# Kernel optimization log

Hardware: AMD Instinct MI355X
Metric: run time of the kernel (lower is better)

## Reference

```python
import jax, jax.numpy as jnp
import numpy as np
from jax import lax


def _viterbi_decode(logits, trans):
    """Batched Viterbi decode (tf.contrib.crf.crf_decode semantics, full lengths).
    logits: [B, T, U] unary potentials; trans: [U, U], trans[i, j] = score(i -> j).
    Returns int32 tags [B, T]."""
    logits_t = jnp.swapaxes(logits, 0, 1)  # [T, B, U]
    init_v = logits_t[0]                   # [B, U]

    def fwd_step(v, logit_t):
        # scores[b, i, j] = v[b, i] + trans[i, j]
        scores = v[:, :, None] + trans[None, :, :]          # [B, U, U]
        bp = jnp.argmax(scores, axis=1).astype(jnp.int32)   # [B, U] best prev tag
        v_new = jnp.max(scores, axis=1) + logit_t           # [B, U]
        return v_new, bp

    v_last, bps = lax.scan(fwd_step, init_v, logits_t[1:])  # bps: [T-1, B, U]
    last_tag = jnp.argmax(v_last, axis=1).astype(jnp.int32)  # [B]

    def bwd_step(tag, bp):
        # tag is the tag at t+1; bp[b, k] = best tag at t given tag k at t+1
        new_tag = jnp.take_along_axis(bp, tag[:, None], axis=1)[:, 0]
        return new_tag, new_tag

    _, tags_prefix = lax.scan(bwd_step, last_tag, bps, reverse=True)  # [T-1, B]
    tags = jnp.concatenate([tags_prefix, last_tag[None, :]], axis=0)  # [T, B]
    return jnp.swapaxes(tags, 0, 1)  # [B, T]


def setup_inputs() -> dict:
    key = jax.random.key(0)
    k0, k1, k2, k3, k4 = jax.random.split(key, 5)
    B, T, D, U = 64, 512, 1024, 128
    x = jax.random.normal(k0, (B, T, D), dtype=jnp.float32)
    kernel = jax.random.normal(k1, (D, U), dtype=jnp.float32) * (1.0 / np.sqrt(D))
    bias = jnp.zeros((U,), dtype=jnp.float32)
    chain_kernel = jax.random.normal(k2, (U, U), dtype=jnp.float32) * 0.1
    left_boundary = jax.random.normal(k3, (U,), dtype=jnp.float32) * 0.1
    right_boundary = jax.random.normal(k4, (U,), dtype=jnp.float32) * 0.1
    return {
        "x": x,
        "kernel": kernel,
        "bias": bias,
        "chain_kernel": chain_kernel,
        "left_boundary": left_boundary,
        "right_boundary": right_boundary,
    }


def reference(x, kernel, bias, chain_kernel, left_boundary, right_boundary):
    # _dense_layer: linear activation, x @ kernel + bias
    logits = jnp.einsum("btd,du->btu", x, kernel) + bias  # [B, T, U]
    # add_boundary_energy with mask=None: boundaries on first / last timestep
    logits = logits.at[:, 0, :].add(left_boundary)
    logits = logits.at[:, -1, :].add(right_boundary)
    # test_mode='viterbi', learn_mode='join': return decoded tags cast to float32
    tags = _viterbi_decode(logits, chain_kernel)
    return tags.astype(jnp.float32)
```

## Files before the change

kernel.cpp:

```cpp
#include <hip/hip_runtime.h>

#define T_SEQ 512
#define U_TAGS 128
#define D_DIM 1024

__global__ __launch_bounds__(256) void crf_gemm(
    const float* __restrict__ A, const float* __restrict__ Bk,
    const float* __restrict__ bias, const float* __restrict__ lb,
    const float* __restrict__ rb, float* __restrict__ C) {
  __shared__ float As[16][132];
  __shared__ float Bs[16][132];
  const int tid = threadIdx.x;
  const int tx = tid & 15, ty = tid >> 4;
  const int row0 = blockIdx.x * 128;

  const int am = tid >> 2, ak = (tid & 3) << 2;
  const int bk = tid >> 5, bn = (tid & 31) << 2;

  float acc[8][8] = {};

  float4 a0 = *(const float4*)&A[(size_t)(row0 + am) * D_DIM + ak];
  float4 a1 = *(const float4*)&A[(size_t)(row0 + am + 64) * D_DIM + ak];
  float4 b0 = *(const float4*)&Bk[(size_t)bk * U_TAGS + bn];
  float4 b1 = *(const float4*)&Bk[(size_t)(bk + 8) * U_TAGS + bn];

  for (int k0 = 0; k0 < D_DIM; k0 += 16) {
    As[ak + 0][am] = a0.x; As[ak + 1][am] = a0.y;
    As[ak + 2][am] = a0.z; As[ak + 3][am] = a0.w;
    As[ak + 0][am + 64] = a1.x; As[ak + 1][am + 64] = a1.y;
    As[ak + 2][am + 64] = a1.z; As[ak + 3][am + 64] = a1.w;
    *(float4*)&Bs[bk][bn] = b0;
    *(float4*)&Bs[bk + 8][bn] = b1;
    __syncthreads();
    if (k0 + 16 < D_DIM) {
      a0 = *(const float4*)&A[(size_t)(row0 + am) * D_DIM + k0 + 16 + ak];
      a1 = *(const float4*)&A[(size_t)(row0 + am + 64) * D_DIM + k0 + 16 + ak];
      b0 = *(const float4*)&Bk[(size_t)(k0 + 16 + bk) * U_TAGS + bn];
      b1 = *(const float4*)&Bk[(size_t)(k0 + 16 + bk + 8) * U_TAGS + bn];
    }
#pragma unroll
    for (int kk = 0; kk < 16; ++kk) {
      float a[8], b[8];
      *(float4*)&a[0] = *(const float4*)&As[kk][ty * 8];
      *(float4*)&a[4] = *(const float4*)&As[kk][ty * 8 + 4];
      *(float4*)&b[0] = *(const float4*)&Bs[kk][tx * 8];
      *(float4*)&b[4] = *(const float4*)&Bs[kk][tx * 8 + 4];
#pragma unroll
      for (int r = 0; r < 8; ++r)
#pragma unroll
        for (int c = 0; c < 8; ++c) acc[r][c] = fmaf(a[r], b[c], acc[r][c]);
    }
    __syncthreads();
  }

#pragma unroll
  for (int r = 0; r < 8; ++r) {
    const int row = row0 + ty * 8 + r;
    const int t = row & (T_SEQ - 1);
    float o[8];
#pragma unroll
    for (int c = 0; c < 8; ++c) {
      float v = acc[r][c] + bias[tx * 8 + c];
      if (t == 0) v += lb[tx * 8 + c];
      if (t == T_SEQ - 1) v += rb[tx * 8 + c];
      o[c] = v;
    }
    *(float4*)&C[(size_t)row * U_TAGS + tx * 8] = *(float4*)&o[0];
    *(float4*)&C[(size_t)row * U_TAGS + tx * 8 + 4] = *(float4*)&o[4];
  }
}

__device__ __forceinline__ float fmax_dpp1(float m) {
  int i = __builtin_amdgcn_mov_dpp(__float_as_int(m), 0xB1, 0xF, 0xF, true);
  return fmaxf(m, __int_as_float(i));
}
__device__ __forceinline__ float fmax_dpp2(float m) {
  int i = __builtin_amdgcn_mov_dpp(__float_as_int(m), 0x4E, 0xF, 0xF, true);
  return fmaxf(m, __int_as_float(i));
}
__device__ __forceinline__ int imin_dpp1(int v) {
  int i = __builtin_amdgcn_mov_dpp(v, 0xB1, 0xF, 0xF, true);
  return v < i ? v : i;
}
__device__ __forceinline__ int imin_dpp2(int v) {
  int i = __builtin_amdgcn_mov_dpp(v, 0x4E, 0xF, 0xF, true);
  return v < i ? v : i;
}

__global__ __launch_bounds__(512) void crf_viterbi(
    const float* __restrict__ logits,
    const float* __restrict__ trans,
    float* __restrict__ out) {
  __shared__ __align__(16) float vbuf[2][U_TAGS];
  __shared__ __align__(16) unsigned char bp[T_SEQ * U_TAGS];
  __shared__ unsigned char tags[T_SEQ];
  __shared__ float red_v[8];
  __shared__ int red_i[8];

  const int b = blockIdx.x;
  const int tid = threadIdx.x;
  const int j = tid >> 2;
  const int seg = tid & 3;
  const float* lg_b = logits + (size_t)b * T_SEQ * U_TAGS;

  float* tstage = (float*)bp;
#pragma unroll
  for (int it = 0; it < 8; ++it)
    *(float4*)&tstage[(it * 512 + tid) * 4] =
        *(const float4*)&trans[(it * 512 + tid) * 4];
  __syncthreads();
  float tr[32];
#pragma unroll
  for (int e = 0; e < 32; ++e) tr[e] = tstage[(seg * 32 + e) * U_TAGS + j];
  if (tid < U_TAGS) vbuf[0][tid] = lg_b[tid];
  __syncthreads();

  float lg = lg_b[U_TAGS + j];
  for (int t = 1; t < T_SEQ; ++t) {
    float lg_next = (t < T_SEQ - 1) ? lg_b[(size_t)(t + 1) * U_TAGS + j] : 0.0f;
    const float* vcur = &vbuf[(t - 1) & 1][seg * 32];
    float s[32];
#pragma unroll
    for (int q = 0; q < 8; ++q) {
      float4 vv = *(const float4*)&vcur[q * 4];
      s[q * 4 + 0] = vv.x + tr[q * 4 + 0];
      s[q * 4 + 1] = vv.y + tr[q * 4 + 1];
      s[q * 4 + 2] = vv.z + tr[q * 4 + 2];
      s[q * 4 + 3] = vv.w + tr[q * 4 + 3];
    }
    float m0 = s[0], m1 = s[1], m2 = s[2], m3 = s[3];
#pragma unroll
    for (int e = 4; e < 32; e += 4) {
      m0 = fmaxf(m0, s[e + 0]); m1 = fmaxf(m1, s[e + 1]);
      m2 = fmaxf(m2, s[e + 2]); m3 = fmaxf(m3, s[e + 3]);
    }
    float m = fmaxf(fmaxf(m0, m1), fmaxf(m2, m3));
    m = fmax_dpp1(m);
    m = fmax_dpp2(m);
    int el = 64;
#pragma unroll
    for (int e = 31; e >= 0; --e) el = (s[e] == m) ? e : el;
    int ic = (el < 64) ? (seg * 32 + el) : 1023;
    ic = imin_dpp1(ic);
    ic = imin_dpp2(ic);
    if (seg == 0) {
      vbuf[t & 1][j] = m + lg;
      bp[(t - 1) * U_TAGS + j] = (unsigned char)ic;
    }
    __syncthreads();
    lg = lg_next;
  }

  if (tid < U_TAGS) {
    float val = vbuf[(T_SEQ - 1) & 1][tid];
    int idx = tid;
#pragma unroll
    for (int off = 1; off < 64; off <<= 1) {
      float vo = __shfl_xor(val, off);
      int io = __shfl_xor(idx, off);
      if (vo > val || (vo == val && io < idx)) { val = vo; idx = io; }
    }
    if ((tid & 63) == 0) { red_v[tid >> 6] = val; red_i[tid >> 6] = idx; }
  }
  __syncthreads();
  if (tid == 0) {
    int tg = (red_v[1] > red_v[0]) ? red_i[1] : red_i[0];
    tags[T_SEQ - 1] = (unsigned char)tg;
    for (int t = T_SEQ - 2; t >= 0; --t) {
      tg = bp[t * U_TAGS + tg];
      tags[t] = (unsigned char)tg;
    }
  }
  __syncthreads();
  out[(size_t)b * T_SEQ + tid] = (float)tags[tid];
}

extern "C" void kernel_launch(void* const* d_in, const int* in_sizes, int n_in,
                              void* d_out, int out_size, void* d_ws,
                              size_t ws_size, hipStream_t stream) {
  const float* x = (const float*)d_in[0];
  const float* kern = (const float*)d_in[1];
  const float* bias = (const float*)d_in[2];
  const float* chain = (const float*)d_in[3];
  const float* lb = (const float*)d_in[4];
  const float* rb = (const float*)d_in[5];
  float* out = (float*)d_out;
  float* logits = (float*)d_ws;

  crf_gemm<<<256, 256, 0, stream>>>(x, kern, bias, lb, rb, logits);
  crf_viterbi<<<64, 512, 0, stream>>>(logits, chain, out);
}
```

Measured before the change: 614.9 us.

## Parallelize Viterbi backtrack by segments and cut LDS conflicts in recurrence

The serial single-thread backtrack becomes a segmented parallel scheme. Each of 8 waves composes the backpointer maps over its 64-step segment for all 128 tags. The segment seeds are then chained and each segment is replayed in parallel. The forward loop also replicates the score vector per segment to avoid LDS bank conflicts, uses max3 trees and split argmin chains, prefetches logits two steps ahead, and swaps __syncthreads for an LDS-only barrier. The GEMM B-fragment layout is interleaved to reduce shared-memory bank conflicts. The segmented backtrack does 128 times more pointer chasing per segment, and the custom barrier depends on the global loads needing no vmcnt wait.

```diff
diff --git a/kernel.cpp b/kernel.cpp
--- a/kernel.cpp
+++ b/kernel.cpp
@@ -43,8 +43,8 @@
       float a[8], b[8];
       *(float4*)&a[0] = *(const float4*)&As[kk][ty * 8];
       *(float4*)&a[4] = *(const float4*)&As[kk][ty * 8 + 4];
-      *(float4*)&b[0] = *(const float4*)&Bs[kk][tx * 8];
-      *(float4*)&b[4] = *(const float4*)&Bs[kk][tx * 8 + 4];
+      *(float4*)&b[0] = *(const float4*)&Bs[kk][tx * 4];
+      *(float4*)&b[4] = *(const float4*)&Bs[kk][tx * 4 + 64];
 #pragma unroll
       for (int r = 0; r < 8; ++r)
 #pragma unroll
@@ -57,19 +57,30 @@
   for (int r = 0; r < 8; ++r) {
     const int row = row0 + ty * 8 + r;
     const int t = row & (T_SEQ - 1);
+    const int n0 = tx * 4, n1 = tx * 4 + 64;
     float o[8];
 #pragma unroll
-    for (int c = 0; c < 8; ++c) {
-      float v = acc[r][c] + bias[tx * 8 + c];
-      if (t == 0) v += lb[tx * 8 + c];
-      if (t == T_SEQ - 1) v += rb[tx * 8 + c];
+    for (int c = 0; c < 4; ++c) {
+      float v = acc[r][c] + bias[n0 + c];
+      if (t == 0) v += lb[n0 + c];
+      if (t == T_SEQ - 1) v += rb[n0 + c];
       o[c] = v;
     }
-    *(float4*)&C[(size_t)row * U_TAGS + tx * 8] = *(float4*)&o[0];
-    *(float4*)&C[(size_t)row * U_TAGS + tx * 8 + 4] = *(float4*)&o[4];
-  }
-}
-
+#pragma unroll
+    for (int c = 0; c < 4; ++c) {
+      float v = acc[r][c + 4] + bias[n1 + c];
+      if (t == 0) v += lb[n1 + c];
+      if (t == T_SEQ - 1) v += rb[n1 + c];
+      o[c + 4] = v;
+    }
+    *(float4*)&C[(size_t)row * U_TAGS + n0] = *(float4*)&o[0];
+    *(float4*)&C[(size_t)row * U_TAGS + n1] = *(float4*)&o[4];
+  }
+}
+
+__device__ __forceinline__ void barrier_lds_only() {
+  asm volatile("s_waitcnt lgkmcnt(0)\n\ts_barrier" ::: "memory");
+}
 __device__ __forceinline__ float fmax_dpp1(float m) {
   int i = __builtin_amdgcn_mov_dpp(__float_as_int(m), 0xB1, 0xF, 0xF, true);
   return fmaxf(m, __int_as_float(i));
@@ -85,15 +96,20 @@
 __device__ __forceinline__ int imin_dpp2(int v) {
   int i = __builtin_amdgcn_mov_dpp(v, 0x4E, 0xF, 0xF, true);
   return v < i ? v : i;
+}
+__device__ __forceinline__ float max3f(float a, float b, float c) {
+  return fmaxf(fmaxf(a, b), c);
 }
 
 __global__ __launch_bounds__(512) void crf_viterbi(
     const float* __restrict__ logits,
     const float* __restrict__ trans,
     float* __restrict__ out) {
-  __shared__ __align__(16) float vbuf[2][U_TAGS];
+  __shared__ __align__(16) float vbuf[2][4][136];
   __shared__ __align__(16) unsigned char bp[T_SEQ * U_TAGS];
   __shared__ unsigned char tags[T_SEQ];
+  __shared__ unsigned char M[8][U_TAGS];
+  __shared__ int seedL[8];
   __shared__ float red_v[8];
   __shared__ int red_i[8];
 
@@ -112,47 +128,65 @@
   float tr[32];
 #pragma unroll
   for (int e = 0; e < 32; ++e) tr[e] = tstage[(seg * 32 + e) * U_TAGS + j];
-  if (tid < U_TAGS) vbuf[0][tid] = lg_b[tid];
-  __syncthreads();
-
-  float lg = lg_b[U_TAGS + j];
+  if (tid < U_TAGS) {
+    float v0 = lg_b[tid];
+#pragma unroll
+    for (int cp = 0; cp < 4; ++cp) vbuf[0][cp][tid] = v0;
+  }
+  __syncthreads();
+
+  float lgp0 = lg_b[1 * U_TAGS + j];
+  float lgp1 = lg_b[2 * U_TAGS + j];
   for (int t = 1; t < T_SEQ; ++t) {
-    float lg_next = (t < T_SEQ - 1) ? lg_b[(size_t)(t + 1) * U_TAGS + j] : 0.0f;
-    const float* vcur = &vbuf[(t - 1) & 1][seg * 32];
+    int tp = t + 2; if (tp > T_SEQ - 1) tp = T_SEQ - 1;
+    float lgnew = lg_b[(size_t)tp * U_TAGS + j];
+
+    const float* vrow = &vbuf[(t - 1) & 1][seg][seg * 32];
     float s[32];
 #pragma unroll
     for (int q = 0; q < 8; ++q) {
-      float4 vv = *(const float4*)&vcur[q * 4];
+      float4 vv = *(const float4*)&vrow[q * 4];
       s[q * 4 + 0] = vv.x + tr[q * 4 + 0];
       s[q * 4 + 1] = vv.y + tr[q * 4 + 1];
       s[q * 4 + 2] = vv.z + tr[q * 4 + 2];
       s[q * 4 + 3] = vv.w + tr[q * 4 + 3];
     }
-    float m0 = s[0], m1 = s[1], m2 = s[2], m3 = s[3];
-#pragma unroll
-    for (int e = 4; e < 32; e += 4) {
-      m0 = fmaxf(m0, s[e + 0]); m1 = fmaxf(m1, s[e + 1]);
-      m2 = fmaxf(m2, s[e + 2]); m3 = fmaxf(m3, s[e + 3]);
-    }
-    float m = fmaxf(fmaxf(m0, m1), fmaxf(m2, m3));
+    float a0 = max3f(s[0], s[1], s[2]),   a1 = max3f(s[3], s[4], s[5]);
+    float a2 = max3f(s[6], s[7], s[8]),   a3 = max3f(s[9], s[10], s[11]);
+    float a4 = max3f(s[12], s[13], s[14]), a5 = max3f(s[15], s[16], s[17]);
+    float a6 = max3f(s[18], s[19], s[20]), a7 = max3f(s[21], s[22], s[23]);
+    float a8 = max3f(s[24], s[25], s[26]), a9 = max3f(s[27], s[28], s[29]);
+    float a10 = fmaxf(s[30], s[31]);
+    float b0 = max3f(a0, a1, a2), b1 = max3f(a3, a4, a5);
+    float b2 = max3f(a6, a7, a8), b3 = fmaxf(a9, a10);
+    float m = fmaxf(max3f(b0, b1, b2), b3);
     m = fmax_dpp1(m);
     m = fmax_dpp2(m);
-    int el = 64;
-#pragma unroll
-    for (int e = 31; e >= 0; --e) el = (s[e] == m) ? e : el;
-    int ic = (el < 64) ? (seg * 32 + el) : 1023;
+    int e0 = 127, e1 = 127, e2 = 127, e3 = 127;
+#pragma unroll
+    for (int e = 7; e >= 0; --e) {
+      e0 = (s[e] == m) ? e : e0;
+      e1 = (s[8 + e] == m) ? 8 + e : e1;
+      e2 = (s[16 + e] == m) ? 16 + e : e2;
+      e3 = (s[24 + e] == m) ? 24 + e : e3;
+    }
+    int el = min(min(e0, e1), min(e2, e3));
+    int ic = (el < 127) ? seg * 32 + el : 1023;
     ic = imin_dpp1(ic);
     ic = imin_dpp2(ic);
     if (seg == 0) {
-      vbuf[t & 1][j] = m + lg;
+      float vn = m + lgp0;
+#pragma unroll
+      for (int cp = 0; cp < 4; ++cp) vbuf[t & 1][cp][j] = vn;
       bp[(t - 1) * U_TAGS + j] = (unsigned char)ic;
     }
-    __syncthreads();
-    lg = lg_next;
+    lgp0 = lgp1;
+    lgp1 = lgnew;
+    barrier_lds_only();
   }
 
   if (tid < U_TAGS) {
-    float val = vbuf[(T_SEQ - 1) & 1][tid];
+    float val = vbuf[1][0][tid];
     int idx = tid;
 #pragma unroll
     for (int off = 1; off < 64; off <<= 1) {
@@ -166,9 +200,33 @@
   if (tid == 0) {
     int tg = (red_v[1] > red_v[0]) ? red_i[1] : red_i[0];
     tags[T_SEQ - 1] = (unsigned char)tg;
-    for (int t = T_SEQ - 2; t >= 0; --t) {
-      tg = bp[t * U_TAGS + tg];
-      tags[t] = (unsigned char)tg;
+  }
+  __syncthreads();
+
+  const int w = tid >> 6, l = tid & 63;
+  const int lo = w * 64;
+  const int hi = (w == 7) ? (T_SEQ - 2) : (w * 64 + 63);
+  {
+    int c0 = l, c1 = l + 64;
+    for (int t = hi; t >= lo; --t) {
+      c0 = bp[t * U_TAGS + c0];
+      c1 = bp[t * U_TAGS + c1];
+    }
+    M[w][l] = (unsigned char)c0;
+    M[w][l + 64] = (unsigned char)c1;
+  }
+  __syncthreads();
+  if (tid == 0) {
+    int sd = tags[T_SEQ - 1];
+    seedL[7] = sd;
+    for (int w2 = 7; w2 >= 1; --w2) { sd = M[w2][sd]; seedL[w2 - 1] = sd; }
+  }
+  __syncthreads();
+  if (l == 0) {
+    int cur = seedL[w];
+    for (int t = hi; t >= lo; --t) {
+      cur = bp[t * U_TAGS + cur];
+      tags[t] = (unsigned char)cur;
     }
   }
   __syncthreads();
```

Result: faster. 602.3 us (-2.0%).
